# Kernel optimization log

Measured on AMD Instinct MI355X. Metric: run time of the kernel, lower is better.

Reference implementation:

```python
import jax, jax.numpy as jnp
import numpy as np

N_NODES = 50000
N_EDGES = 1600000
IN_DIM = 6
HID = 128
OUT = 128
N_LAYERS = 3
N_EXPERTS = 4
N_GRAPHS = 16
LOGN_SCALE = float(np.log(1e4))  # normalizes log(graph size) into ~[0,1]


def setup_inputs() -> dict:
    key = jax.random.key(0)
    ks = jax.random.split(key, 10)
    x = jax.random.normal(ks[0], (N_NODES, IN_DIM), dtype=jnp.float32)
    edge_index = jax.random.randint(ks[1], (2, N_EDGES), 0, N_NODES, dtype=jnp.int64)
    batch = jnp.sort(jax.random.randint(ks[2], (N_NODES,), 0, N_GRAPHS, dtype=jnp.int64))
    s = 1.0 / np.sqrt(HID)
    W_enc = jax.random.normal(ks[3], (IN_DIM, HID), dtype=jnp.float32) / np.sqrt(IN_DIM)
    b_enc = jnp.zeros((HID,), dtype=jnp.float32)
    # per-expert, per-layer GraphConv weights (hidden->hidden ... hidden->out; dims equal here)
    W_self = jax.random.normal(ks[4], (N_EXPERTS, N_LAYERS, HID, OUT), dtype=jnp.float32) * s
    W_nbr = jax.random.normal(ks[5], (N_EXPERTS, N_LAYERS, HID, OUT), dtype=jnp.float32) * s
    b_conv = jnp.zeros((N_EXPERTS, N_LAYERS, OUT), dtype=jnp.float32)
    centers = jnp.linspace(0.0, 1.0, N_EXPERTS, dtype=jnp.float32)
    return {"x": x, "edge_index": edge_index, "batch": batch, "W_enc": W_enc,
            "b_enc": b_enc, "W_self": W_self, "W_nbr": W_nbr, "b_conv": b_conv,
            "centers": centers}


def _expert(h, src, dst, Ws, Wn, b):
    # Ws, Wn: [L, H, H]; b: [L, H]
    for l in range(N_LAYERS):
        agg = jax.ops.segment_sum(h[src], dst, num_segments=N_NODES)  # gather+scatter
        h = h @ Ws[l] + agg @ Wn[l] + b[l]
        if l < N_LAYERS - 1:
            h = jax.nn.relu(h)
    return h


def reference(x, edge_index, batch, W_enc, b_enc, W_self, W_nbr, b_conv, centers):
    src, dst = edge_index[0], edge_index[1]
    h = jax.nn.relu(x @ W_enc + b_enc)  # SharedBusEncoder
    # graph size features: normalized log(#nodes per graph), per node
    counts = jax.ops.segment_sum(jnp.ones((N_NODES,), jnp.float32), batch,
                                 num_segments=N_GRAPHS)
    logn = jnp.log(jnp.maximum(counts, 1.0))[batch] / LOGN_SCALE  # [N]
    probs = jax.nn.softmax(-(logn[:, None] - centers[None, :]) ** 2, axis=-1)  # [N, E]
    y = jax.vmap(_expert, in_axes=(None, None, None, 0, 0, 0))(
        h, src, dst, W_self, W_nbr, b_conv)  # [E, N, OUT]
    return jnp.einsum('enh,ne->nh', y, probs)
```

## Files before the change

kernel.cpp:

```cpp
#include <hip/hip_runtime.h>

#define NN 50000
#define NE 1600000
#define NG 16
#define HID 128
#define NEXP 4
#define LOGN_SCALE 9.210340371976184f

#define NBUK 256
#define NPB  196
#define NBLK 128
#define EPB  ((NE + NBLK - 1)/NBLK)
#define MAXB 16384

typedef unsigned short u16;
typedef unsigned int u32;
typedef unsigned char u8;
typedef __attribute__((ext_vector_type(8))) short short8b;
typedef __attribute__((ext_vector_type(4))) float f32x4;
typedef __attribute__((ext_vector_type(2))) float f32x2;

static __device__ __forceinline__ u16 f2bf(float f){
  union { float f; u32 i; } c; c.f = f;
  return (u16)((c.i + 0x7fffu + ((c.i>>16)&1u)) >> 16);
}
static __device__ __forceinline__ u8 f2fp8(float v){
  return (u8)(__builtin_amdgcn_cvt_pk_fp8_f32(v, v, 0, false) & 0xffu);
}
static __device__ __forceinline__ short8b fp8x8_to_bf16(uint2 v){
  f32x2 a = __builtin_amdgcn_cvt_pk_f32_fp8(v.x, false);
  f32x2 b = __builtin_amdgcn_cvt_pk_f32_fp8(v.x, true);
  f32x2 c = __builtin_amdgcn_cvt_pk_f32_fp8(v.y, false);
  f32x2 d = __builtin_amdgcn_cvt_pk_f32_fp8(v.y, true);
  short8b t;
  t[0]=(short)f2bf(a.x); t[1]=(short)f2bf(a.y);
  t[2]=(short)f2bf(b.x); t[3]=(short)f2bf(b.y);
  t[4]=(short)f2bf(c.x); t[5]=(short)f2bf(c.y);
  t[6]=(short)f2bf(d.x); t[7]=(short)f2bf(d.y);
  return t;
}

__global__ void k_bounds(const int* __restrict__ batch, int* __restrict__ gstart){
  int g = threadIdx.x;
  if(g > NG) return;
  int lo = 0, hi = NN;
  while(lo < hi){ int mid = (lo+hi)>>1; if(batch[mid] < g) lo = mid+1; else hi = mid; }
  gstart[g] = lo;
}

__global__ void k_probs(const int* __restrict__ batch, const int* __restrict__ gstart,
                        const float* __restrict__ centers, float* __restrict__ probs){
  int n = blockIdx.x*blockDim.x + threadIdx.x;
  if(n >= NN) return;
  int b = batch[n];
  float c = (float)(gstart[b+1] - gstart[b]);
  float logn = logf(fmaxf(c, 1.f)) * (1.f/LOGN_SCALE);
  float s[NEXP]; float m = -1e30f;
  #pragma unroll
  for(int e=0;e<NEXP;e++){ float d = logn - centers[e]; s[e] = -d*d; m = fmaxf(m, s[e]); }
  float sum = 0.f;
  #pragma unroll
  for(int e=0;e<NEXP;e++){ s[e] = expf(s[e]-m); sum += s[e]; }
  float inv = 1.f/sum;
  #pragma unroll
  for(int e=0;e<NEXP;e++) probs[n*NEXP+e] = s[e]*inv;
}

__global__ void k_enc(const float* __restrict__ x, const float* __restrict__ Wenc,
                      const float* __restrict__ benc, u8* __restrict__ h08, float esc){
  int t = blockIdx.x*blockDim.x + threadIdx.x;
  if(t >= NN*HID) return;
  int n = t >> 7, j = t & 127;
  float acc = benc[j];
  #pragma unroll
  for(int k=0;k<6;k++) acc += x[n*6+k]*Wenc[k*HID+j];
  h08[t] = f2fp8(fmaxf(acc, 0.f)*esc);
}

__global__ void k_wcvtT(const float* __restrict__ Wself, const float* __restrict__ Wnbr,
                        u16* __restrict__ WbfT){
  int t = blockIdx.x*blockDim.x + threadIdx.x;
  if(t >= 12*HID*256) return;
  int el = t / (HID*256);
  int r  = t % (HID*256);
  int j  = r >> 8;
  int k  = r & 255;
  float v = (k < HID) ? Wself[(size_t)el*HID*HID + (size_t)k*HID + j]
                      : Wnbr [(size_t)el*HID*HID + (size_t)(k-HID)*HID + j];
  WbfT[t] = f2bf(v);
}

__global__ __launch_bounds__(256) void k_hist(const int* __restrict__ dst,
                                              int* __restrict__ hist){
  __shared__ int h[NBUK];
  for(int i=threadIdx.x; i<NBUK; i+=256) h[i] = 0;
  __syncthreads();
  int e0 = blockIdx.x*EPB, e1 = min(NE, e0 + EPB);
  for(int e = e0 + (int)threadIdx.x; e < e1; e += 256)
    atomicAdd(&h[dst[e]/NPB], 1);
  __syncthreads();
  for(int i=threadIdx.x; i<NBUK; i+=256) hist[blockIdx.x*NBUK + i] = h[i];
}

__global__ __launch_bounds__(1024) void k_hscan(const int* __restrict__ hist,
                                                int* __restrict__ hoff,
                                                int* __restrict__ bbase){
  __shared__ int sd[NBLK*NBUK];
  __shared__ int ps[1024];
  int t = threadIdx.x;
  for(int i=t; i<NBLK*NBUK; i+=1024){
    int bucket = i >> 7;
    int blk = i & (NBLK-1);
    sd[i] = hist[blk*NBUK + bucket];
  }
  __syncthreads();
  int base = t*32, sum = 0;
  #pragma unroll
  for(int i=0;i<32;i++){ int v = sd[base+i]; sd[base+i] = sum; sum += v; }
  ps[t] = sum;
  __syncthreads();
  for(int d=1; d<1024; d<<=1){
    int v = (t>=d) ? ps[t-d] : 0;
    __syncthreads();
    ps[t] += v;
    __syncthreads();
  }
  int add = (t>0) ? ps[t-1] : 0;
  for(int i=base; i<base+32; i++){
    int bucket = i >> 7, blk = i & (NBLK-1);
    int v = sd[i] + add;
    hoff[blk*NBUK + bucket] = v;
    if(blk == 0) bbase[bucket] = v;
  }
  if(t == 1023) bbase[NBUK] = NE;
}

__global__ __launch_bounds__(256) void k_scatter(const int* __restrict__ src,
                                                 const int* __restrict__ dst,
                                                 const int* __restrict__ hoff,
                                                 u32* __restrict__ packed){
  __shared__ u32 ent[EPB];
  __shared__ u32 outp[EPB];
  __shared__ u32 cnt[NBUK], exc[NBUK], cur[NBUK], gb[NBUK];
  int t = threadIdx.x;
  int e0 = blockIdx.x*EPB;
  int len = min(EPB, NE - e0);
  cnt[t] = 0;
  __syncthreads();
  for(int i=t; i<len; i+=256){
    int d = dst[e0+i];
    u32 b = (u32)(d/NPB);
    ent[i] = (u32)src[e0+i] | ((u32)(d - (int)b*NPB) << 16) | (b << 24);
    atomicAdd(&cnt[b], 1u);
  }
  __syncthreads();
  u32 c = cnt[t];
  exc[t] = c;
  __syncthreads();
  for(int d=1; d<256; d<<=1){
    u32 v = (t>=(u32)d) ? exc[t-d] : 0u;
    __syncthreads();
    exc[t] += v;
    __syncthreads();
  }
  u32 excl = exc[t] - c;
  cur[t] = excl;
  gb[t] = (u32)hoff[blockIdx.x*NBUK + t];
  __syncthreads();
  exc[t] = excl;
  __syncthreads();
  for(int i=t; i<len; i+=256){
    u32 v = ent[i];
    u32 p = atomicAdd(&cur[v>>24], 1u);
    outp[p] = v;
  }
  __syncthreads();
  for(int i=t; i<len; i+=256){
    u32 v = outp[i];
    u32 b = v >> 24;
    packed[gb[b] + ((u32)i - exc[b])] = v & 0x00ffffffu;
  }
}

__global__ __launch_bounds__(256) void k_build(const u32* __restrict__ packed,
                                               const int* __restrict__ bbase,
                                               int* __restrict__ offs,
                                               u16* __restrict__ srcs16){
  __shared__ u32 ent[MAXB];
  __shared__ u16 outb[MAXB];
  __shared__ u32 cnt[256], exc[256], cur[256];
  int b = blockIdx.x, t = threadIdx.x;
  int e0 = bbase[b], e1 = bbase[b+1];
  int len = e1 - e0, cap = min(len, MAXB);
  for(int i=t; i<cap; i+=256) ent[i] = packed[e0+i];
  cnt[t] = 0;
  __syncthreads();
  for(int i=t; i<len; i+=256){
    u32 v = (i < MAXB) ? ent[i] : packed[e0+i];
    atomicAdd(&cnt[(v>>16)&0xffu], 1u);
  }
  __syncthreads();
  u32 c = cnt[t];
  exc[t] = c;
  __syncthreads();
  for(int d=1; d<256; d<<=1){
    u32 v = (t>=(u32)d) ? exc[t-d] : 0u;
    __syncthreads();
    exc[t] += v;
    __syncthreads();
  }
  u32 excl = exc[t] - c;
  int node = b*NPB + t;
  if(t < NPB && node < NN) offs[node] = e0 + (int)excl;
  cur[t] = excl;
  if(b == NBUK-1 && t == 0) offs[NN] = NE;
  __syncthreads();
  for(int i=t; i<len; i+=256){
    u32 v = (i < MAXB) ? ent[i] : packed[e0+i];
    u32 p = atomicAdd(&cur[(v>>16)&0xffu], 1u);
    u16 sv = (u16)(v & 0xffffu);
    if(p < (u32)MAXB) outb[p] = sv;
    else srcs16[e0+p] = sv;
  }
  __syncthreads();
  for(int i=t; i<cap; i+=256) srcs16[e0+i] = outb[i];
}

template<int TW, bool RELU, bool LAST>
__global__ __launch_bounds__(256) void k_fused(
    const u8* __restrict__ tin, const int* __restrict__ offs,
    const u16* __restrict__ srcs, const u16* __restrict__ WbfT,
    const float* __restrict__ bconv, int layer,
    const float* __restrict__ probs,
    u8* __restrict__ tout, float* __restrict__ outp,
    float bias_fold, float store_fold)
{
  constexpr int BPL = TW/64;
  __shared__ u16 G[16*TW];
  int wave = threadIdx.x>>6, lane = threadIdx.x&63;
  int l16 = lane&15, lq = lane>>4;
  int n0 = blockIdx.x*16;

  const u8* hbase = tin + lane*BPL;
  for(int i=0;i<4;i++){
    int row = wave*4 + i;
    int node = n0 + row;
    float acc[BPL];
    #pragma unroll
    for(int b=0;b<BPL;b++) acc[b]=0.f;
    if(node < NN){
      int beg = offs[node], end = offs[node+1];
      for(int eb=beg; eb<end; eb+=64){
        int idx = eb + lane;
        int s = (idx < end) ? (int)srcs[idx] : 0;
        int cnt = min(64, end-eb);
        int j = 0;
        if(BPL == 8){
          for(; j+8<=cnt; j+=8){
            uint2 v[8];
            #pragma unroll
            for(int u=0;u<8;u++){
              int sj = __shfl(s, j+u, 64);
              v[u] = *(const uint2*)(hbase + (size_t)sj*TW);
            }
            #pragma unroll
            for(int u=0;u<8;u++){
              f32x2 f0 = __builtin_amdgcn_cvt_pk_f32_fp8(v[u].x, false);
              f32x2 f1 = __builtin_amdgcn_cvt_pk_f32_fp8(v[u].x, true);
              f32x2 f2 = __builtin_amdgcn_cvt_pk_f32_fp8(v[u].y, false);
              f32x2 f3 = __builtin_amdgcn_cvt_pk_f32_fp8(v[u].y, true);
              acc[0]+=f0.x; acc[1]+=f0.y; acc[2]+=f1.x; acc[3]+=f1.y;
              acc[4]+=f2.x; acc[5]+=f2.y; acc[6]+=f3.x; acc[7]+=f3.y;
            }
          }
          for(; j<cnt; j++){
            int sj = __shfl(s, j, 64);
            uint2 v = *(const uint2*)(hbase + (size_t)sj*TW);
            f32x2 f0 = __builtin_amdgcn_cvt_pk_f32_fp8(v.x, false);
            f32x2 f1 = __builtin_amdgcn_cvt_pk_f32_fp8(v.x, true);
            f32x2 f2 = __builtin_amdgcn_cvt_pk_f32_fp8(v.y, false);
            f32x2 f3 = __builtin_amdgcn_cvt_pk_f32_fp8(v.y, true);
            acc[0]+=f0.x; acc[1]+=f0.y; acc[2]+=f1.x; acc[3]+=f1.y;
            acc[4]+=f2.x; acc[5]+=f2.y; acc[6]+=f3.x; acc[7]+=f3.y;
          }
        } else {
          for(; j+8<=cnt; j+=8){
            u32 v[8];
            #pragma unroll
            for(int u=0;u<8;u++){
              int sj = __shfl(s, j+u, 64);
              v[u] = *(const u16*)(hbase + (size_t)sj*TW);
            }
            #pragma unroll
            for(int u=0;u<8;u++){
              f32x2 f0 = __builtin_amdgcn_cvt_pk_f32_fp8(v[u], false);
              acc[0]+=f0.x; acc[1]+=f0.y;
            }
          }
          for(; j<cnt; j++){
            int sj = __shfl(s, j, 64);
            u32 v = *(const u16*)(hbase + (size_t)sj*TW);
            f32x2 f0 = __builtin_amdgcn_cvt_pk_f32_fp8(v, false);
            acc[0]+=f0.x; acc[1]+=f0.y;
          }
        }
      }
    }
    u32 boff = (u32)(lane*BPL*2) ^ (u32)((row&7)<<4);
    u16* gp = (u16*)((char*)G + (size_t)row*(TW*2) + boff);
    if(BPL == 8){
      short8b tv;
      #pragma unroll
      for(int b=0;b<8;b++) tv[b] = (short)f2bf(acc[b]);
      *(short8b*)gp = tv;
    } else {
      gp[0] = f2bf(acc[0]); gp[1] = f2bf(acc[1]);
    }
  }
  __syncthreads();

  if(!LAST){
    int e = wave;
    const u16* WT = WbfT + (size_t)((e*3+layer)*HID)*256;
    const int eoff = (TW==512) ? e*128 : 0;
    short8b Af[8];
    int na = n0 + l16; if(na > NN-1) na = NN-1;
    const u8* srow = tin + (size_t)na*TW;
    #pragma unroll
    for(int ks=0; ks<4; ks++)
      Af[ks] = fp8x8_to_bf16(*(const uint2*)(srow + eoff + ks*32 + lq*8));
    int row = l16;
    #pragma unroll
    for(int ks=4; ks<8; ks++){
      u32 boff = (u32)((eoff + (ks-4)*32 + lq*8)*2) ^ (u32)((row&7)<<4);
      Af[ks] = *(const short8b*)((char*)G + (size_t)row*(TW*2) + boff);
    }
    const float* bias = bconv + (e*3+layer)*HID;
    #pragma unroll 1
    for(int ct=0; ct<8; ct++){
      f32x4 binit = *(const f32x4*)(bias + ct*16 + lq*4);
      f32x4 acc;
      #pragma unroll
      for(int r=0;r<4;r++) acc[r] = binit[r]*bias_fold;
      const u16* wp = WT + (size_t)(ct*16 + l16)*256 + lq*8;
      #pragma unroll
      for(int ks=0; ks<8; ks++){
        short8b Bf = *(const short8b*)(wp + ks*32);
        acc = __builtin_amdgcn_mfma_f32_16x16x32_bf16(Bf, Af[ks], acc, 0,0,0);
      }
      int n = n0 + l16;
      if(n < NN){
        float v0,v1,v2,v3;
        if(RELU){
          v0=fmaxf(acc[0],0.f)*store_fold; v1=fmaxf(acc[1],0.f)*store_fold;
          v2=fmaxf(acc[2],0.f)*store_fold; v3=fmaxf(acc[3],0.f)*store_fold;
        } else {
          v0=acc[0]*store_fold; v1=acc[1]*store_fold;
          v2=acc[2]*store_fold; v3=acc[3]*store_fold;
        }
        u32 wv = __builtin_amdgcn_cvt_pk_fp8_f32(v0, v1, 0, false);
        wv = __builtin_amdgcn_cvt_pk_fp8_f32(v2, v3, wv, true);
        *(u32*)(tout + (size_t)n*512 + e*128 + ct*16 + lq*4) = wv;
      }
    }
  } else {
    int cs = wave*32;
    f32x4 tot[2];
    #pragma unroll
    for(int ct=0;ct<2;ct++){
      #pragma unroll
      for(int r=0;r<4;r++) tot[ct][r] = 0.f;
    }
    int na = n0 + l16; if(na > NN-1) na = NN-1;
    float pv[4];
    #pragma unroll
    for(int e=0;e<4;e++) pv[e] = probs[na*NEXP + e];
    const u8* srow = tin + (size_t)na*TW;
    int row = l16;
    #pragma unroll 1
    for(int e=0;e<4;e++){
      const u16* WT = WbfT + (size_t)((e*3+layer)*HID)*256;
      const int eoff = e*128;
      short8b Af[8];
      #pragma unroll
      for(int ks=0; ks<4; ks++)
        Af[ks] = fp8x8_to_bf16(*(const uint2*)(srow + eoff + ks*32 + lq*8));
      #pragma unroll
      for(int ks=4; ks<8; ks++){
        u32 boff = (u32)((eoff + (ks-4)*32 + lq*8)*2) ^ (u32)((row&7)<<4);
        Af[ks] = *(const short8b*)((char*)G + (size_t)row*(TW*2) + boff);
      }
      const float* bias = bconv + (e*3+layer)*HID;
      #pragma unroll
      for(int ct=0; ct<2; ct++){
        int cb = cs + ct*16;
        f32x4 binit = *(const f32x4*)(bias + cb + lq*4);
        f32x4 acc;
        #pragma unroll
        for(int r=0;r<4;r++) acc[r] = binit[r]*bias_fold;
        const u16* wp = WT + (size_t)(cb + l16)*256 + lq*8;
        #pragma unroll
        for(int ks=0; ks<8; ks++){
          short8b Bf = *(const short8b*)(wp + ks*32);
          acc = __builtin_amdgcn_mfma_f32_16x16x32_bf16(Bf, Af[ks], acc, 0,0,0);
        }
        float s0 = pv[e]*store_fold;
        #pragma unroll
        for(int r=0;r<4;r++) tot[ct][r] += s0*acc[r];
      }
    }
    int n = n0 + l16;
    if(n < NN){
      #pragma unroll
      for(int ct=0; ct<2; ct++)
        *(f32x4*)(outp + (size_t)n*HID + cs + ct*16 + lq*4) = tot[ct];
    }
  }
}

extern "C" void kernel_launch(void* const* d_in, const int* in_sizes, int n_in,
                              void* d_out, int out_size, void* d_ws, size_t ws_size,
                              hipStream_t stream){
  const float* x      = (const float*)d_in[0];
  const int*   eidx   = (const int*)d_in[1];
  const int*   batch  = (const int*)d_in[2];
  const float* Wenc   = (const float*)d_in[3];
  const float* benc   = (const float*)d_in[4];
  const float* Wself  = (const float*)d_in[5];
  const float* Wnbr   = (const float*)d_in[6];
  const float* bconv  = (const float*)d_in[7];
  const float* centers= (const float*)d_in[8];
  float* out = (float*)d_out;
  const int* src = eidx;
  const int* dst = eidx + NE;

  char* w = (char*)d_ws;
  size_t off = 0;
  auto alloc = [&](size_t b)->char*{ char* p = w + off; off = (off + b + 255) & ~(size_t)255; return p; };

  u8*  h08   = (u8*)alloc((size_t)NN*HID);
  u8*  hA8   = (u8*)alloc((size_t)NN*NEXP*HID);
  u8*  hB8   = (u8*)alloc((size_t)NN*NEXP*HID);
  u16* WbfT  = (u16*)alloc((size_t)12*HID*256*2);
  float* probs = (float*)alloc((size_t)NN*NEXP*4);
  int* gstart = (int*)alloc(256);
  int* offs  = (int*)alloc((size_t)(NN+1)*4);
  u32* packed= (u32*)alloc((size_t)NE*4);
  u16* srcs16= (u16*)alloc((size_t)NE*2);
  int* hist  = (int*)alloc((size_t)NBLK*NBUK*4);
  int* hoff  = (int*)alloc((size_t)NBLK*NBUK*4);
  int* bbase = (int*)alloc((size_t)(NBUK+1)*4);
  if(off > ws_size) return;

  k_bounds<<<1, 32, 0, stream>>>(batch, gstart);
  k_probs<<<(NN+255)/256, 256, 0, stream>>>(batch, gstart, centers, probs);
  k_enc<<<(NN*HID+255)/256, 256, 0, stream>>>(x, Wenc, benc, h08, 0.5f);
  k_wcvtT<<<(12*HID*256+255)/256, 256, 0, stream>>>(Wself, Wnbr, WbfT);

  k_hist<<<NBLK, 256, 0, stream>>>(dst, hist);
  k_hscan<<<1, 1024, 0, stream>>>(hist, hoff, bbase);
  k_scatter<<<NBLK, 256, 0, stream>>>(src, dst, hoff, packed);
  k_build<<<NBUK, 256, 0, stream>>>(packed, bbase, offs, srcs16);

  int nblocks = (NN + 15)/16;
  k_fused<128,true,false><<<nblocks, 256, 0, stream>>>(
      h08, offs, srcs16, WbfT, bconv, 0, nullptr, hA8, nullptr, 0.5f, 0.125f);
  k_fused<512,true,false><<<nblocks, 256, 0, stream>>>(
      hA8, offs, srcs16, WbfT, bconv, 1, nullptr, hB8, nullptr, 0.0625f, 0.5f);
  k_fused<512,false,true><<<nblocks, 256, 0, stream>>>(
      hB8, offs, srcs16, WbfT, bconv, 2, probs, nullptr, out, 0.03125f, 32.0f);
}
```

Before: 642.8 us.

## Split fused aggregate+GEMM kernel into separate aggregation and GEMM kernels

Each layer's fused kernel, which gathered neighbour features into LDS and then ran the MFMA GEMM, is split into two kernels. One does the neighbour aggregation with one wave per node and writes bf16 sums to a global buffer. The other loads those sums from global memory as its A-operand and runs the GEMM. This removes the LDS staging and the block-wide barrier so gather and GEMM can each run at their own occupancy. In exchange, each layer writes and reads an extra bf16 intermediate of up to NN*512*2 bytes and adds kernel launches.

```diff
diff --git a/kernel.cpp b/kernel.cpp
--- a/kernel.cpp
+++ b/kernel.cpp
@@ -226,115 +226,106 @@
   for(int i=t; i<cap; i+=256) srcs16[e0+i] = outb[i];
 }
 
+template<int BPL>
+__global__ __launch_bounds__(256) void k_agg8(const u8* __restrict__ hin,
+                                              const int* __restrict__ offs,
+                                              const u16* __restrict__ srcs,
+                                              u16* __restrict__ hout){
+  const int W = BPL*64;
+  int node = blockIdx.x*4 + (threadIdx.x>>6);
+  if(node >= NN) return;
+  int lane = threadIdx.x & 63;
+  const u8* hbase = hin + lane*BPL;
+  float acc[BPL];
+  #pragma unroll
+  for(int i=0;i<BPL;i++) acc[i] = 0.f;
+  int beg = offs[node], end = offs[node+1];
+  for(int eb=beg; eb<end; eb+=64){
+    int idx = eb + lane;
+    int s = (idx < end) ? (int)srcs[idx] : 0;
+    int cnt = min(64, end-eb);
+    int j = 0;
+    if(BPL == 8){
+      for(; j+8<=cnt; j+=8){
+        uint2 v[8];
+        #pragma unroll
+        for(int u=0;u<8;u++){
+          int sj = __shfl(s, j+u, 64);
+          v[u] = *(const uint2*)(hbase + (size_t)sj*W);
+        }
+        #pragma unroll
+        for(int u=0;u<8;u++){
+          f32x2 f0 = __builtin_amdgcn_cvt_pk_f32_fp8(v[u].x, false);
+          f32x2 f1 = __builtin_amdgcn_cvt_pk_f32_fp8(v[u].x, true);
+          f32x2 f2 = __builtin_amdgcn_cvt_pk_f32_fp8(v[u].y, false);
+          f32x2 f3 = __builtin_amdgcn_cvt_pk_f32_fp8(v[u].y, true);
+          acc[0]+=f0.x; acc[1]+=f0.y; acc[2]+=f1.x; acc[3]+=f1.y;
+          acc[4]+=f2.x; acc[5]+=f2.y; acc[6]+=f3.x; acc[7]+=f3.y;
+        }
+      }
+      for(; j<cnt; j++){
+        int sj = __shfl(s, j, 64);
+        uint2 v = *(const uint2*)(hbase + (size_t)sj*W);
+        f32x2 f0 = __builtin_amdgcn_cvt_pk_f32_fp8(v.x, false);
+        f32x2 f1 = __builtin_amdgcn_cvt_pk_f32_fp8(v.x, true);
+        f32x2 f2 = __builtin_amdgcn_cvt_pk_f32_fp8(v.y, false);
+        f32x2 f3 = __builtin_amdgcn_cvt_pk_f32_fp8(v.y, true);
+        acc[0]+=f0.x; acc[1]+=f0.y; acc[2]+=f1.x; acc[3]+=f1.y;
+        acc[4]+=f2.x; acc[5]+=f2.y; acc[6]+=f3.x; acc[7]+=f3.y;
+      }
+    } else {
+      for(; j+8<=cnt; j+=8){
+        u32 v[8];
+        #pragma unroll
+        for(int u=0;u<8;u++){
+          int sj = __shfl(s, j+u, 64);
+          v[u] = *(const u16*)(hbase + (size_t)sj*W);
+        }
+        #pragma unroll
+        for(int u=0;u<8;u++){
+          f32x2 f0 = __builtin_amdgcn_cvt_pk_f32_fp8(v[u], false);
+          acc[0]+=f0.x; acc[1]+=f0.y;
+        }
+      }
+      for(; j<cnt; j++){
+        int sj = __shfl(s, j, 64);
+        u32 v = *(const u16*)(hbase + (size_t)sj*W);
+        f32x2 f0 = __builtin_amdgcn_cvt_pk_f32_fp8(v, false);
+        acc[0]+=f0.x; acc[1]+=f0.y;
+      }
+    }
+  }
+  u16* o = hout + (size_t)node*W + lane*BPL;
+  #pragma unroll
+  for(int i=0;i<BPL;i++) o[i] = f2bf(acc[i]);
+}
+
 template<int TW, bool RELU, bool LAST>
-__global__ __launch_bounds__(256) void k_fused(
-    const u8* __restrict__ tin, const int* __restrict__ offs,
-    const u16* __restrict__ srcs, const u16* __restrict__ WbfT,
-    const float* __restrict__ bconv, int layer,
+__global__ __launch_bounds__(256) void k_gemm8(
+    const u8* __restrict__ tin, const u16* __restrict__ aggb,
+    const u16* __restrict__ WbfT, const float* __restrict__ bconv, int layer,
     const float* __restrict__ probs,
     u8* __restrict__ tout, float* __restrict__ outp,
     float bias_fold, float store_fold)
 {
-  constexpr int BPL = TW/64;
-  __shared__ u16 G[16*TW];
   int wave = threadIdx.x>>6, lane = threadIdx.x&63;
   int l16 = lane&15, lq = lane>>4;
   int n0 = blockIdx.x*16;
-
-  const u8* hbase = tin + lane*BPL;
-  for(int i=0;i<4;i++){
-    int row = wave*4 + i;
-    int node = n0 + row;
-    float acc[BPL];
-    #pragma unroll
-    for(int b=0;b<BPL;b++) acc[b]=0.f;
-    if(node < NN){
-      int beg = offs[node], end = offs[node+1];
-      for(int eb=beg; eb<end; eb+=64){
-        int idx = eb + lane;
-        int s = (idx < end) ? (int)srcs[idx] : 0;
-        int cnt = min(64, end-eb);
-        int j = 0;
-        if(BPL == 8){
-          for(; j+8<=cnt; j+=8){
-            uint2 v[8];
-            #pragma unroll
-            for(int u=0;u<8;u++){
-              int sj = __shfl(s, j+u, 64);
-              v[u] = *(const uint2*)(hbase + (size_t)sj*TW);
-            }
-            #pragma unroll
-            for(int u=0;u<8;u++){
-              f32x2 f0 = __builtin_amdgcn_cvt_pk_f32_fp8(v[u].x, false);
-              f32x2 f1 = __builtin_amdgcn_cvt_pk_f32_fp8(v[u].x, true);
-              f32x2 f2 = __builtin_amdgcn_cvt_pk_f32_fp8(v[u].y, false);
-              f32x2 f3 = __builtin_amdgcn_cvt_pk_f32_fp8(v[u].y, true);
-              acc[0]+=f0.x; acc[1]+=f0.y; acc[2]+=f1.x; acc[3]+=f1.y;
-              acc[4]+=f2.x; acc[5]+=f2.y; acc[6]+=f3.x; acc[7]+=f3.y;
-            }
-          }
-          for(; j<cnt; j++){
-            int sj = __shfl(s, j, 64);
-            uint2 v = *(const uint2*)(hbase + (size_t)sj*TW);
-            f32x2 f0 = __builtin_amdgcn_cvt_pk_f32_fp8(v.x, false);
-            f32x2 f1 = __builtin_amdgcn_cvt_pk_f32_fp8(v.x, true);
-            f32x2 f2 = __builtin_amdgcn_cvt_pk_f32_fp8(v.y, false);
-            f32x2 f3 = __builtin_amdgcn_cvt_pk_f32_fp8(v.y, true);
-            acc[0]+=f0.x; acc[1]+=f0.y; acc[2]+=f1.x; acc[3]+=f1.y;
-            acc[4]+=f2.x; acc[5]+=f2.y; acc[6]+=f3.x; acc[7]+=f3.y;
-          }
-        } else {
-          for(; j+8<=cnt; j+=8){
-            u32 v[8];
-            #pragma unroll
-            for(int u=0;u<8;u++){
-              int sj = __shfl(s, j+u, 64);
-              v[u] = *(const u16*)(hbase + (size_t)sj*TW);
-            }
-            #pragma unroll
-            for(int u=0;u<8;u++){
-              f32x2 f0 = __builtin_amdgcn_cvt_pk_f32_fp8(v[u], false);
-              acc[0]+=f0.x; acc[1]+=f0.y;
-            }
-          }
-          for(; j<cnt; j++){
-            int sj = __shfl(s, j, 64);
-            u32 v = *(const u16*)(hbase + (size_t)sj*TW);
-            f32x2 f0 = __builtin_amdgcn_cvt_pk_f32_fp8(v, false);
-            acc[0]+=f0.x; acc[1]+=f0.y;
-          }
-        }
-      }
-    }
-    u32 boff = (u32)(lane*BPL*2) ^ (u32)((row&7)<<4);
-    u16* gp = (u16*)((char*)G + (size_t)row*(TW*2) + boff);
-    if(BPL == 8){
-      short8b tv;
-      #pragma unroll
-      for(int b=0;b<8;b++) tv[b] = (short)f2bf(acc[b]);
-      *(short8b*)gp = tv;
-    } else {
-      gp[0] = f2bf(acc[0]); gp[1] = f2bf(acc[1]);
-    }
-  }
-  __syncthreads();
+  int na = n0 + l16; if(na > NN-1) na = NN-1;
+  const u8*  srow = tin  + (size_t)na*TW;
+  const u16* arow = aggb + (size_t)na*TW;
 
   if(!LAST){
     int e = wave;
     const u16* WT = WbfT + (size_t)((e*3+layer)*HID)*256;
     const int eoff = (TW==512) ? e*128 : 0;
     short8b Af[8];
-    int na = n0 + l16; if(na > NN-1) na = NN-1;
-    const u8* srow = tin + (size_t)na*TW;
     #pragma unroll
     for(int ks=0; ks<4; ks++)
       Af[ks] = fp8x8_to_bf16(*(const uint2*)(srow + eoff + ks*32 + lq*8));
-    int row = l16;
     #pragma unroll
-    for(int ks=4; ks<8; ks++){
-      u32 boff = (u32)((eoff + (ks-4)*32 + lq*8)*2) ^ (u32)((row&7)<<4);
-      Af[ks] = *(const short8b*)((char*)G + (size_t)row*(TW*2) + boff);
-    }
+    for(int ks=4; ks<8; ks++)
+      Af[ks] = *(const short8b*)(arow + eoff + (ks-4)*32 + lq*8);
     const float* bias = bconv + (e*3+layer)*HID;
     #pragma unroll 1
     for(int ct=0; ct<8; ct++){
@@ -371,12 +362,9 @@
       #pragma unroll
       for(int r=0;r<4;r++) tot[ct][r] = 0.f;
     }
-    int na = n0 + l16; if(na > NN-1) na = NN-1;
     float pv[4];
     #pragma unroll
     for(int e=0;e<4;e++) pv[e] = probs[na*NEXP + e];
-    const u8* srow = tin + (size_t)na*TW;
-    int row = l16;
     #pragma unroll 1
     for(int e=0;e<4;e++){
       const u16* WT = WbfT + (size_t)((e*3+layer)*HID)*256;
@@ -386,10 +374,8 @@
       for(int ks=0; ks<4; ks++)
         Af[ks] = fp8x8_to_bf16(*(const uint2*)(srow + eoff + ks*32 + lq*8));
       #pragma unroll
-      for(int ks=4; ks<8; ks++){
-        u32 boff = (u32)((eoff + (ks-4)*32 + lq*8)*2) ^ (u32)((row&7)<<4);
-        Af[ks] = *(const short8b*)((char*)G + (size_t)row*(TW*2) + boff);
-      }
+      for(int ks=4; ks<8; ks++)
+        Af[ks] = *(const short8b*)(arow + eoff + (ks-4)*32 + lq*8);
       const float* bias = bconv + (e*3+layer)*HID;
       #pragma unroll
       for(int ct=0; ct<2; ct++){
@@ -441,6 +427,7 @@
   u8*  h08   = (u8*)alloc((size_t)NN*HID);
   u8*  hA8   = (u8*)alloc((size_t)NN*NEXP*HID);
   u8*  hB8   = (u8*)alloc((size_t)NN*NEXP*HID);
+  u16* aggb  = (u16*)alloc((size_t)NN*NEXP*HID*2);
   u16* WbfT  = (u16*)alloc((size_t)12*HID*256*2);
   float* probs = (float*)alloc((size_t)NN*NEXP*4);
   int* gstart = (int*)alloc(256);
@@ -462,11 +449,15 @@
   k_scatter<<<NBLK, 256, 0, stream>>>(src, dst, hoff, packed);
   k_build<<<NBUK, 256, 0, stream>>>(packed, bbase, offs, srcs16);
 
-  int nblocks = (NN + 15)/16;
-  k_fused<128,true,false><<<nblocks, 256, 0, stream>>>(
-      h08, offs, srcs16, WbfT, bconv, 0, nullptr, hA8, nullptr, 0.5f, 0.125f);
-  k_fused<512,true,false><<<nblocks, 256, 0, stream>>>(
-      hA8, offs, srcs16, WbfT, bconv, 1, nullptr, hB8, nullptr, 0.0625f, 0.5f);
-  k_fused<512,false,true><<<nblocks, 256, 0, stream>>>(
-      hB8, offs, srcs16, WbfT, bconv, 2, probs, nullptr, out, 0.03125f, 32.0f);
-}
+  int agrid = (NN+3)/4;
+  int ggrid = (NN+15)/16;
+  k_agg8<2><<<agrid, 256, 0, stream>>>(h08, offs, srcs16, aggb);
+  k_gemm8<128,true,false><<<ggrid, 256, 0, stream>>>(
+      h08, aggb, WbfT, bconv, 0, nullptr, hA8, nullptr, 0.5f, 0.125f);
+  k_agg8<8><<<agrid, 256, 0, stream>>>(hA8, offs, srcs16, aggb);
+  k_gemm8<512,true,false><<<ggrid, 256, 0, stream>>>(
+      hA8, aggb, WbfT, bconv, 1, nullptr, hB8, nullptr, 0.0625f, 0.5f);
+  k_agg8<8><<<agrid, 256, 0, stream>>>(hB8, offs, srcs16, aggb);
+  k_gemm8<512,false,true><<<ggrid, 256, 0, stream>>>(
+      hB8, aggb, WbfT, bconv, 2, probs, nullptr, out, 0.03125f, 32.0f);
+}
```

Result: slower. 716.7 us (+11.5%).
